# Optimization experiments

Measured on AMD Instinct MI355X. Metric: run time of the kernel, lower is better.

## Reference

```python
import jax, jax.numpy as jnp
import numpy as np

B, T, C, HS = 4, 2048, 1024, 64  # batch, seq, n_embd, head_size


def setup_inputs() -> dict:
    key = jax.random.key(0)
    k1, k2, k3, k4 = jax.random.split(key, 4)
    x = jax.random.normal(k1, (B, T, C), dtype=jnp.float32)
    Wq = jax.random.normal(k2, (HS, C), dtype=jnp.float32) * (C ** -0.5)
    Wk = jax.random.normal(k3, (HS, C), dtype=jnp.float32) * (C ** -0.5)
    Wv = jax.random.normal(k4, (HS, C), dtype=jnp.float32) * (C ** -0.5)
    return {"x": x, "Wq": Wq, "Wk": Wk, "Wv": Wv}


def reference(x, Wq, Wk, Wv):
    # q,k,v: [B,T,HS] (nn.Linear: x @ W.T, no bias)
    q = jnp.einsum('btc,hc->bth', x, Wq)
    k = jnp.einsum('btc,hc->bth', x, Wk)
    v = jnp.einsum('btc,hc->bth', x, Wv)
    scale = k.shape[-1] ** -0.5
    wei = jnp.einsum('bth,bsh->bts', q, k) * scale  # [B,T,T]
    # causal mask (tril == 0 -> -inf)
    mask = jnp.tril(jnp.ones((T, T), dtype=bool))
    wei = jnp.where(mask, wei, -jnp.inf)
    wei = jax.nn.softmax(wei, axis=-1)
    # dropout p=0.0 -> identity
    out = jnp.einsum('bts,bsh->bth', wei, v)  # [B,T,HS]
    return out
```

## Files before the change

kernel.cpp:

```cpp
#include <hip/hip_runtime.h>
#include <hip/hip_bf16.h>

#define BB 4
#define TT 2048
#define CC 1024
#define HSZ 64
#define NTOT 8192

typedef __attribute__((ext_vector_type(8))) short bf16x8;
typedef __attribute__((ext_vector_type(4))) float f32x4;

__device__ __forceinline__ unsigned short f2bf(float x) {
    __hip_bfloat16 h = __float2bfloat16(x);
    return *reinterpret_cast<unsigned short*>(&h);
}
__device__ __forceinline__ float bf2f(unsigned short u) {
    return __uint_as_float(((unsigned int)u) << 16);
}

__global__ __launch_bounds__(256) void convert_w(
    const float* __restrict__ Wq, const float* __restrict__ Wk,
    const float* __restrict__ Wv, unsigned short* __restrict__ Wh) {
    int i = blockIdx.x * 256 + threadIdx.x;
    if (i >= 192 * 1024) return;
    int c = i >> 10, kk = i & 1023;
    float val;
    if (c < 64) val = Wq[(size_t)c * CC + kk] * 0.125f;
    else if (c < 128) val = Wk[(size_t)(c - 64) * CC + kk];
    else val = Wv[(size_t)(c - 128) * CC + kk];
    Wh[i] = f2bf(val);
}

__global__ __launch_bounds__(512, 2) void qkv_mfma(
    const float* __restrict__ x, const unsigned short* __restrict__ Wh,
    unsigned short* __restrict__ qs, unsigned short* __restrict__ ksb,
    unsigned short* __restrict__ vT) {
    __shared__ __align__(16) unsigned char smem[110592];
    unsigned short* Wc = (unsigned short*)smem;
    float* Pt = (float*)smem;

    const int tid = threadIdx.x;
    const int w = tid >> 6, lane = tid & 63;
    const int l16 = lane & 15, quad = lane >> 4;
    const int ms = w & 1, ks = w >> 1;
    const int row0 = blockIdx.x * 32;
    const int Arow = row0 + ms * 16 + l16;

    f32x4 acc[12];
#pragma unroll
    for (int t = 0; t < 12; ++t) acc[t] = (f32x4){0.f, 0.f, 0.f, 0.f};

    for (int ch = 0; ch < 4; ++ch) {
        const int kb = ks * 256 + ch * 64;
        __syncthreads();
        {
            const int gt = tid & 127;
            unsigned short* Wck = Wc + ks * 13824;
#pragma unroll
            for (int it = 0; it < 12; ++it) {
                int e = gt + it * 128;
                int c = e >> 3, g = e & 7;
                *(uint4*)&Wck[c * 72 + g * 8] = *(const uint4*)&Wh[(size_t)c * CC + kb + g * 8];
            }
        }
        const float* xp = x + (size_t)Arow * CC + kb;
        float4 xa = *(const float4*)&xp[quad * 8];
        float4 xb = *(const float4*)&xp[quad * 8 + 4];
        float4 xc = *(const float4*)&xp[32 + quad * 8];
        float4 xd = *(const float4*)&xp[32 + quad * 8 + 4];
        bf16x8 ah0, al0, ah1, al1;
        {
            float v0[8] = {xa.x, xa.y, xa.z, xa.w, xb.x, xb.y, xb.z, xb.w};
            float v1[8] = {xc.x, xc.y, xc.z, xc.w, xd.x, xd.y, xd.z, xd.w};
#pragma unroll
            for (int j = 0; j < 8; ++j) {
                unsigned short h = f2bf(v0[j]);
                ah0[j] = (short)h;
                al0[j] = (short)f2bf(v0[j] - bf2f(h));
                unsigned short h2 = f2bf(v1[j]);
                ah1[j] = (short)h2;
                al1[j] = (short)f2bf(v1[j] - bf2f(h2));
            }
        }
        __syncthreads();
        const unsigned short* Wck = Wc + ks * 13824;
#pragma unroll
        for (int nt = 0; nt < 12; ++nt) {
            bf16x8 b0 = *(const bf16x8*)&Wck[(nt * 16 + l16) * 72 + quad * 8];
            bf16x8 b1 = *(const bf16x8*)&Wck[(nt * 16 + l16) * 72 + 32 + quad * 8];
            f32x4 a = acc[nt];
            a = __builtin_amdgcn_mfma_f32_16x16x32_bf16(ah0, b0, a, 0, 0, 0);
            a = __builtin_amdgcn_mfma_f32_16x16x32_bf16(al0, b0, a, 0, 0, 0);
            a = __builtin_amdgcn_mfma_f32_16x16x32_bf16(ah1, b1, a, 0, 0, 0);
            a = __builtin_amdgcn_mfma_f32_16x16x32_bf16(al1, b1, a, 0, 0, 0);
            acc[nt] = a;
        }
    }
    __syncthreads();
#pragma unroll
    for (int nt = 0; nt < 12; ++nt)
#pragma unroll
        for (int r = 0; r < 4; ++r)
            Pt[((ms * 4 + ks) * 16 + quad * 4 + r) * 196 + nt * 16 + l16] = acc[nt][r];
    __syncthreads();
    for (int e = tid; e < 32 * 192; e += 512) {
        int row = e / 192, col = e - row * 192;
        int m2 = row >> 4, r16 = row & 15;
        float s = 0.f;
#pragma unroll
        for (int kk = 0; kk < 4; ++kk) s += Pt[((m2 * 4 + kk) * 16 + r16) * 196 + col];
        unsigned short h = f2bf(s);
        int grow = row0 + row;
        if (col < 64) qs[(size_t)grow * HSZ + col] = h;
        else if (col < 128) ksb[(size_t)grow * HSZ + (col - 64)] = h;
        else vT[(size_t)(col - 128) * NTOT + grow] = h;
    }
}

__global__ __launch_bounds__(256, 2) void attn_mfma(
    const unsigned short* __restrict__ qs, const unsigned short* __restrict__ ksb,
    const unsigned short* __restrict__ vT, float* __restrict__ out) {
    __shared__ __align__(16) unsigned char smem[18688];
    unsigned short* Ps = (unsigned short*)smem;
    float* Om = (float*)smem;
    float* Lm = (float*)(smem + 17408);

    const int raw = blockIdx.x;
    const int i = (raw < 256) ? raw : 767 - raw;
    const int b = i >> 7;
    const int qt = i & 127;
    const int t0 = qt * 16;
    const int tid = threadIdx.x;
    const int w = tid >> 6, lane = tid & 63;
    const int l16 = lane & 15, quad = lane >> 4;

    const size_t qoff = (size_t)(b * TT + t0 + l16) * HSZ + quad * 8;
    const bf16x8 aq0 = *(const bf16x8*)&qs[qoff];
    const bf16x8 aq1 = *(const bf16x8*)&qs[qoff + 32];

    f32x4 OC[4];
#pragma unroll
    for (int t = 0; t < 4; ++t) OC[t] = (f32x4){0.f, 0.f, 0.f, 0.f};
    float lsum[4] = {0.f, 0.f, 0.f, 0.f};

    const int nk = (qt >> 2) + 1;
    for (int j = w; j < nk; j += 4) {
        const int key0 = j * 64;
        f32x4 S[4];
#pragma unroll
        for (int nt = 0; nt < 4; ++nt) {
            const size_t ko = (size_t)(b * TT + key0 + nt * 16 + l16) * HSZ + quad * 8;
            bf16x8 bk0 = *(const bf16x8*)&ksb[ko];
            bf16x8 bk1 = *(const bf16x8*)&ksb[ko + 32];
            f32x4 a = (f32x4){0.f, 0.f, 0.f, 0.f};
            a = __builtin_amdgcn_mfma_f32_16x16x32_bf16(aq0, bk0, a, 0, 0, 0);
            a = __builtin_amdgcn_mfma_f32_16x16x32_bf16(aq1, bk1, a, 0, 0, 0);
            S[nt] = a;
        }
        if (j == nk - 1) {
#pragma unroll
            for (int nt = 0; nt < 4; ++nt) {
                const int key = key0 + nt * 16 + l16;
#pragma unroll
                for (int r = 0; r < 4; ++r)
                    if (key > t0 + quad * 4 + r) S[nt][r] = -1e30f;
            }
        }
#pragma unroll
        for (int nt = 0; nt < 4; ++nt)
#pragma unroll
            for (int r = 0; r < 4; ++r) S[nt][r] = __expf(S[nt][r]);
#pragma unroll
        for (int r = 0; r < 4; ++r)
            lsum[r] += S[0][r] + S[1][r] + S[2][r] + S[3][r];
        unsigned short* Pw = Ps + w * 1152;
#pragma unroll
        for (int nt = 0; nt < 4; ++nt)
#pragma unroll
            for (int r = 0; r < 4; ++r)
                Pw[(quad * 4 + r) * 72 + nt * 16 + l16] = f2bf(S[nt][r]);
        bf16x8 pf0 = *(const bf16x8*)&Pw[l16 * 72 + quad * 8];
        bf16x8 pf1 = *(const bf16x8*)&Pw[l16 * 72 + 32 + quad * 8];
#pragma unroll
        for (int ht = 0; ht < 4; ++ht) {
            const size_t vo = (size_t)(ht * 16 + l16) * NTOT + b * TT + key0 + quad * 8;
            bf16x8 bv0 = *(const bf16x8*)&vT[vo];
            bf16x8 bv1 = *(const bf16x8*)&vT[vo + 32];
            f32x4 a = OC[ht];
            a = __builtin_amdgcn_mfma_f32_16x16x32_bf16(pf0, bv0, a, 0, 0, 0);
            a = __builtin_amdgcn_mfma_f32_16x16x32_bf16(pf1, bv1, a, 0, 0, 0);
            OC[ht] = a;
        }
    }
#pragma unroll
    for (int r = 0; r < 4; ++r) {
        float v = lsum[r];
#pragma unroll
        for (int off = 1; off < 16; off <<= 1) v += __shfl_xor(v, off, 64);
        lsum[r] = v;
    }
    __syncthreads();
#pragma unroll
    for (int ht = 0; ht < 4; ++ht)
#pragma unroll
        for (int r = 0; r < 4; ++r)
            Om[(w * 16 + quad * 4 + r) * 68 + ht * 16 + l16] = OC[ht][r];
    if (l16 == 0) {
#pragma unroll
        for (int r = 0; r < 4; ++r) Lm[w * 16 + quad * 4 + r] = lsum[r];
    }
    __syncthreads();
    {
        const int row = tid >> 4, h0 = (tid & 15) * 4;
        float L = 0.f, o0 = 0.f, o1 = 0.f, o2 = 0.f, o3 = 0.f;
#pragma unroll
        for (int w2 = 0; w2 < 4; ++w2) {
            L += Lm[w2 * 16 + row];
            const float* p = &Om[(w2 * 16 + row) * 68 + h0];
            o0 += p[0]; o1 += p[1]; o2 += p[2]; o3 += p[3];
        }
        const float inv = 1.f / L;
        *(float4*)&out[(size_t)(b * TT + t0 + row) * HSZ + h0] =
            (float4){o0 * inv, o1 * inv, o2 * inv, o3 * inv};
    }
}

extern "C" void kernel_launch(void* const* d_in, const int* in_sizes, int n_in,
                              void* d_out, int out_size, void* d_ws, size_t ws_size,
                              hipStream_t stream) {
    const float* x  = (const float*)d_in[0];
    const float* Wq = (const float*)d_in[1];
    const float* Wk = (const float*)d_in[2];
    const float* Wv = (const float*)d_in[3];
    float* out = (float*)d_out;

    unsigned short* qs = (unsigned short*)d_ws;
    unsigned short* ksb = qs + (size_t)NTOT * HSZ;
    unsigned short* vT = ksb + (size_t)NTOT * HSZ;
    unsigned short* Wh = vT + (size_t)NTOT * HSZ;

    convert_w<<<768, 256, 0, stream>>>(Wq, Wk, Wv, Wh);
    qkv_mfma<<<256, 512, 0, stream>>>(x, Wh, qs, ksb, vT);
    attn_mfma<<<512, 256, 0, stream>>>(qs, ksb, vT, out);
}
```

Before: 112.2 us.

## Drop LDS weight staging in QKV projection and prefetch K/V in attention

The QKV projection kernel no longer stages weight chunks through shared memory. Each wave reads bf16 weights directly from global/L2, and blocks shrink to 16 rows and 256 threads with twice as many blocks, which removes two barriers per chunk and a large LDS allocation and should allow more occupancy. The attention kernel loads K fragments for the next key tile one iteration ahead and issues V loads before the QK MFMAs, hiding global load latency at the cost of more registers. The attention kernel's shared buffer is also trimmed.

```diff
diff --git a/kernel.cpp b/kernel.cpp
--- a/kernel.cpp
+++ b/kernel.cpp
@@ -31,38 +31,25 @@
     Wh[i] = f2bf(val);
 }
 
-__global__ __launch_bounds__(512, 2) void qkv_mfma(
+__global__ __launch_bounds__(256, 2) void qkv_mfma(
     const float* __restrict__ x, const unsigned short* __restrict__ Wh,
     unsigned short* __restrict__ qs, unsigned short* __restrict__ ksb,
     unsigned short* __restrict__ vT) {
-    __shared__ __align__(16) unsigned char smem[110592];
-    unsigned short* Wc = (unsigned short*)smem;
-    float* Pt = (float*)smem;
+    __shared__ __align__(16) float Pt[4 * 16 * 196];
 
     const int tid = threadIdx.x;
     const int w = tid >> 6, lane = tid & 63;
     const int l16 = lane & 15, quad = lane >> 4;
-    const int ms = w & 1, ks = w >> 1;
-    const int row0 = blockIdx.x * 32;
-    const int Arow = row0 + ms * 16 + l16;
+    const int row0 = blockIdx.x * 16;
+    const int Arow = row0 + l16;
 
     f32x4 acc[12];
 #pragma unroll
     for (int t = 0; t < 12; ++t) acc[t] = (f32x4){0.f, 0.f, 0.f, 0.f};
 
+#pragma unroll
     for (int ch = 0; ch < 4; ++ch) {
-        const int kb = ks * 256 + ch * 64;
-        __syncthreads();
-        {
-            const int gt = tid & 127;
-            unsigned short* Wck = Wc + ks * 13824;
-#pragma unroll
-            for (int it = 0; it < 12; ++it) {
-                int e = gt + it * 128;
-                int c = e >> 3, g = e & 7;
-                *(uint4*)&Wck[c * 72 + g * 8] = *(const uint4*)&Wh[(size_t)c * CC + kb + g * 8];
-            }
-        }
+        const int kb = w * 256 + ch * 64;
         const float* xp = x + (size_t)Arow * CC + kb;
         float4 xa = *(const float4*)&xp[quad * 8];
         float4 xb = *(const float4*)&xp[quad * 8 + 4];
@@ -82,12 +69,11 @@
                 al1[j] = (short)f2bf(v1[j] - bf2f(h2));
             }
         }
-        __syncthreads();
-        const unsigned short* Wck = Wc + ks * 13824;
 #pragma unroll
         for (int nt = 0; nt < 12; ++nt) {
-            bf16x8 b0 = *(const bf16x8*)&Wck[(nt * 16 + l16) * 72 + quad * 8];
-            bf16x8 b1 = *(const bf16x8*)&Wck[(nt * 16 + l16) * 72 + 32 + quad * 8];
+            const unsigned short* Wp = &Wh[(size_t)(nt * 16 + l16) * CC + kb + quad * 8];
+            bf16x8 b0 = *(const bf16x8*)Wp;
+            bf16x8 b1 = *(const bf16x8*)(Wp + 32);
             f32x4 a = acc[nt];
             a = __builtin_amdgcn_mfma_f32_16x16x32_bf16(ah0, b0, a, 0, 0, 0);
             a = __builtin_amdgcn_mfma_f32_16x16x32_bf16(al0, b0, a, 0, 0, 0);
@@ -96,21 +82,19 @@
             acc[nt] = a;
         }
     }
+#pragma unroll
+    for (int nt = 0; nt < 12; ++nt)
+#pragma unroll
+        for (int r = 0; r < 4; ++r)
+            Pt[(w * 16 + quad * 4 + r) * 196 + nt * 16 + l16] = acc[nt][r];
     __syncthreads();
-#pragma unroll
-    for (int nt = 0; nt < 12; ++nt)
-#pragma unroll
-        for (int r = 0; r < 4; ++r)
-            Pt[((ms * 4 + ks) * 16 + quad * 4 + r) * 196 + nt * 16 + l16] = acc[nt][r];
-    __syncthreads();
-    for (int e = tid; e < 32 * 192; e += 512) {
-        int row = e / 192, col = e - row * 192;
-        int m2 = row >> 4, r16 = row & 15;
+    for (int e = tid; e < 16 * 192; e += 256) {
+        const int row = e / 192, col = e - row * 192;
         float s = 0.f;
 #pragma unroll
-        for (int kk = 0; kk < 4; ++kk) s += Pt[((m2 * 4 + kk) * 16 + r16) * 196 + col];
+        for (int kk = 0; kk < 4; ++kk) s += Pt[(kk * 16 + row) * 196 + col];
         unsigned short h = f2bf(s);
-        int grow = row0 + row;
+        const int grow = row0 + row;
         if (col < 64) qs[(size_t)grow * HSZ + col] = h;
         else if (col < 128) ksb[(size_t)grow * HSZ + (col - 64)] = h;
         else vT[(size_t)(col - 128) * NTOT + grow] = h;
@@ -120,7 +104,7 @@
 __global__ __launch_bounds__(256, 2) void attn_mfma(
     const unsigned short* __restrict__ qs, const unsigned short* __restrict__ ksb,
     const unsigned short* __restrict__ vT, float* __restrict__ out) {
-    __shared__ __align__(16) unsigned char smem[18688];
+    __shared__ __align__(16) unsigned char smem[17664];
     unsigned short* Ps = (unsigned short*)smem;
     float* Om = (float*)smem;
     float* Lm = (float*)(smem + 17408);
@@ -143,18 +127,46 @@
     for (int t = 0; t < 4; ++t) OC[t] = (f32x4){0.f, 0.f, 0.f, 0.f};
     float lsum[4] = {0.f, 0.f, 0.f, 0.f};
 
+    const unsigned short* kbase = ksb + (size_t)b * TT * HSZ;
     const int nk = (qt >> 2) + 1;
+
+    bf16x8 ck0[4], ck1[4];
+    if (w < nk) {
+        const int key0 = w * 64;
+#pragma unroll
+        for (int nt = 0; nt < 4; ++nt) {
+            const unsigned short* kp = kbase + (size_t)(key0 + nt * 16 + l16) * HSZ + quad * 8;
+            ck0[nt] = *(const bf16x8*)kp;
+            ck1[nt] = *(const bf16x8*)(kp + 32);
+        }
+    }
+
     for (int j = w; j < nk; j += 4) {
         const int key0 = j * 64;
+        bf16x8 cv0[4], cv1[4];
+#pragma unroll
+        for (int ht = 0; ht < 4; ++ht) {
+            const unsigned short* vp = vT + (size_t)(ht * 16 + l16) * NTOT + b * TT + key0 + quad * 8;
+            cv0[ht] = *(const bf16x8*)vp;
+            cv1[ht] = *(const bf16x8*)(vp + 32);
+        }
+        bf16x8 nk0[4], nk1[4];
+        const bool more = (j + 4) < nk;
+        if (more) {
+            const int key0n = key0 + 256;
+#pragma unroll
+            for (int nt = 0; nt < 4; ++nt) {
+                const unsigned short* kp = kbase + (size_t)(key0n + nt * 16 + l16) * HSZ + quad * 8;
+                nk0[nt] = *(const bf16x8*)kp;
+                nk1[nt] = *(const bf16x8*)(kp + 32);
+            }
+        }
         f32x4 S[4];
 #pragma unroll
         for (int nt = 0; nt < 4; ++nt) {
-            const size_t ko = (size_t)(b * TT + key0 + nt * 16 + l16) * HSZ + quad * 8;
-            bf16x8 bk0 = *(const bf16x8*)&ksb[ko];
-            bf16x8 bk1 = *(const bf16x8*)&ksb[ko + 32];
             f32x4 a = (f32x4){0.f, 0.f, 0.f, 0.f};
-            a = __builtin_amdgcn_mfma_f32_16x16x32_bf16(aq0, bk0, a, 0, 0, 0);
-            a = __builtin_amdgcn_mfma_f32_16x16x32_bf16(aq1, bk1, a, 0, 0, 0);
+            a = __builtin_amdgcn_mfma_f32_16x16x32_bf16(aq0, ck0[nt], a, 0, 0, 0);
+            a = __builtin_amdgcn_mfma_f32_16x16x32_bf16(aq1, ck1[nt], a, 0, 0, 0);
             S[nt] = a;
         }
         if (j == nk - 1) {
@@ -183,13 +195,14 @@
         bf16x8 pf1 = *(const bf16x8*)&Pw[l16 * 72 + 32 + quad * 8];
 #pragma unroll
         for (int ht = 0; ht < 4; ++ht) {
-            const size_t vo = (size_t)(ht * 16 + l16) * NTOT + b * TT + key0 + quad * 8;
-            bf16x8 bv0 = *(const bf16x8*)&vT[vo];
-            bf16x8 bv1 = *(const bf16x8*)&vT[vo + 32];
             f32x4 a = OC[ht];
-            a = __builtin_amdgcn_mfma_f32_16x16x32_bf16(pf0, bv0, a, 0, 0, 0);
-            a = __builtin_amdgcn_mfma_f32_16x16x32_bf16(pf1, bv1, a, 0, 0, 0);
+            a = __builtin_amdgcn_mfma_f32_16x16x32_bf16(pf0, cv0[ht], a, 0, 0, 0);
+            a = __builtin_amdgcn_mfma_f32_16x16x32_bf16(pf1, cv1[ht], a, 0, 0, 0);
             OC[ht] = a;
+        }
+        if (more) {
+#pragma unroll
+            for (int nt = 0; nt < 4; ++nt) { ck0[nt] = nk0[nt]; ck1[nt] = nk1[nt]; }
         }
     }
 #pragma unroll
@@ -240,6 +253,6 @@
     unsigned short* Wh = vT + (size_t)NTOT * HSZ;
 
     convert_w<<<768, 256, 0, stream>>>(Wq, Wk, Wv, Wh);
-    qkv_mfma<<<256, 512, 0, stream>>>(x, Wh, qs, ksb, vT);
+    qkv_mfma<<<512, 256, 0, stream>>>(x, Wh, qs, ksb, vT);
     attn_mfma<<<512, 256, 0, stream>>>(qs, ksb, vT, out);
 }
```

Measured after the change: 120.4 us. 1.07x slower.

## Pre-split x into bf16 hi/lo, drop LDS from QKV GEMM, pair attention key blocks

Applied to the files above, without the earlier changes.

A new conversion kernel splits all of x into bf16 high and low halves in global memory, alongside the weight conversion. The QKV projection is rewritten without shared memory: each wave computes one 16x16 output tile over the full reduction dimension, reading the pre-split x and weights straight from global memory. This removes the LDS staging and the cross-wave split-K reduction. The attention loop now processes two 64-key blocks per iteration to expose more MFMA and load parallelism. The trade-off is an extra full-size write and read of x in bf16, plus higher register pressure in attention.

```diff
diff --git a/kernel.cpp b/kernel.cpp
--- a/kernel.cpp
+++ b/kernel.cpp
@@ -18,109 +18,82 @@
     return __uint_as_float(((unsigned int)u) << 16);
 }
 
-__global__ __launch_bounds__(256) void convert_w(
+__global__ __launch_bounds__(256) void convert_all(
     const float* __restrict__ Wq, const float* __restrict__ Wk,
-    const float* __restrict__ Wv, unsigned short* __restrict__ Wh) {
-    int i = blockIdx.x * 256 + threadIdx.x;
-    if (i >= 192 * 1024) return;
-    int c = i >> 10, kk = i & 1023;
-    float val;
-    if (c < 64) val = Wq[(size_t)c * CC + kk] * 0.125f;
-    else if (c < 128) val = Wk[(size_t)(c - 64) * CC + kk];
-    else val = Wv[(size_t)(c - 128) * CC + kk];
-    Wh[i] = f2bf(val);
-}
-
-__global__ __launch_bounds__(512, 2) void qkv_mfma(
-    const float* __restrict__ x, const unsigned short* __restrict__ Wh,
+    const float* __restrict__ Wv, const float* __restrict__ x,
+    unsigned short* __restrict__ Wh, unsigned short* __restrict__ xh,
+    unsigned short* __restrict__ xl) {
+    const int idx = blockIdx.x * 256 + threadIdx.x;
+    const int stride = 2048 * 256;
+    for (int i = idx; i < 49152; i += stride) {
+        const int c = i >> 8, k4 = i & 255;
+        float4 wv;
+        if (c < 64) {
+            wv = *(const float4*)&Wq[(size_t)c * CC + k4 * 4];
+            wv.x *= 0.125f; wv.y *= 0.125f; wv.z *= 0.125f; wv.w *= 0.125f;
+        } else if (c < 128) {
+            wv = *(const float4*)&Wk[(size_t)(c - 64) * CC + k4 * 4];
+        } else {
+            wv = *(const float4*)&Wv[(size_t)(c - 128) * CC + k4 * 4];
+        }
+        ushort4 h = {f2bf(wv.x), f2bf(wv.y), f2bf(wv.z), f2bf(wv.w)};
+        *(ushort4*)&Wh[(size_t)i * 4] = h;
+    }
+    for (int i = idx; i < 2097152; i += stride) {
+        float4 xv = *(const float4*)&x[(size_t)i * 4];
+        ushort4 h = {f2bf(xv.x), f2bf(xv.y), f2bf(xv.z), f2bf(xv.w)};
+        ushort4 l = {f2bf(xv.x - bf2f(h.x)), f2bf(xv.y - bf2f(h.y)),
+                     f2bf(xv.z - bf2f(h.z)), f2bf(xv.w - bf2f(h.w))};
+        *(ushort4*)&xh[(size_t)i * 4] = h;
+        *(ushort4*)&xl[(size_t)i * 4] = l;
+    }
+}
+
+__global__ __launch_bounds__(768, 4) void qkv_mfma(
+    const unsigned short* __restrict__ xh, const unsigned short* __restrict__ xl,
+    const unsigned short* __restrict__ Wh,
     unsigned short* __restrict__ qs, unsigned short* __restrict__ ksb,
     unsigned short* __restrict__ vT) {
-    __shared__ __align__(16) unsigned char smem[110592];
-    unsigned short* Wc = (unsigned short*)smem;
-    float* Pt = (float*)smem;
-
     const int tid = threadIdx.x;
     const int w = tid >> 6, lane = tid & 63;
     const int l16 = lane & 15, quad = lane >> 4;
-    const int ms = w & 1, ks = w >> 1;
-    const int row0 = blockIdx.x * 32;
-    const int Arow = row0 + ms * 16 + l16;
-
-    f32x4 acc[12];
-#pragma unroll
-    for (int t = 0; t < 12; ++t) acc[t] = (f32x4){0.f, 0.f, 0.f, 0.f};
-
-    for (int ch = 0; ch < 4; ++ch) {
-        const int kb = ks * 256 + ch * 64;
-        __syncthreads();
-        {
-            const int gt = tid & 127;
-            unsigned short* Wck = Wc + ks * 13824;
-#pragma unroll
-            for (int it = 0; it < 12; ++it) {
-                int e = gt + it * 128;
-                int c = e >> 3, g = e & 7;
-                *(uint4*)&Wck[c * 72 + g * 8] = *(const uint4*)&Wh[(size_t)c * CC + kb + g * 8];
-            }
-        }
-        const float* xp = x + (size_t)Arow * CC + kb;
-        float4 xa = *(const float4*)&xp[quad * 8];
-        float4 xb = *(const float4*)&xp[quad * 8 + 4];
-        float4 xc = *(const float4*)&xp[32 + quad * 8];
-        float4 xd = *(const float4*)&xp[32 + quad * 8 + 4];
-        bf16x8 ah0, al0, ah1, al1;
-        {
-            float v0[8] = {xa.x, xa.y, xa.z, xa.w, xb.x, xb.y, xb.z, xb.w};
-            float v1[8] = {xc.x, xc.y, xc.z, xc.w, xd.x, xd.y, xd.z, xd.w};
-#pragma unroll
-            for (int j = 0; j < 8; ++j) {
-                unsigned short h = f2bf(v0[j]);
-                ah0[j] = (short)h;
-                al0[j] = (short)f2bf(v0[j] - bf2f(h));
-                unsigned short h2 = f2bf(v1[j]);
-                ah1[j] = (short)h2;
-                al1[j] = (short)f2bf(v1[j] - bf2f(h2));
-            }
-        }
-        __syncthreads();
-        const unsigned short* Wck = Wc + ks * 13824;
-#pragma unroll
-        for (int nt = 0; nt < 12; ++nt) {
-            bf16x8 b0 = *(const bf16x8*)&Wck[(nt * 16 + l16) * 72 + quad * 8];
-            bf16x8 b1 = *(const bf16x8*)&Wck[(nt * 16 + l16) * 72 + 32 + quad * 8];
-            f32x4 a = acc[nt];
-            a = __builtin_amdgcn_mfma_f32_16x16x32_bf16(ah0, b0, a, 0, 0, 0);
-            a = __builtin_amdgcn_mfma_f32_16x16x32_bf16(al0, b0, a, 0, 0, 0);
-            a = __builtin_amdgcn_mfma_f32_16x16x32_bf16(ah1, b1, a, 0, 0, 0);
-            a = __builtin_amdgcn_mfma_f32_16x16x32_bf16(al1, b1, a, 0, 0, 0);
-            acc[nt] = a;
-        }
-    }
-    __syncthreads();
-#pragma unroll
-    for (int nt = 0; nt < 12; ++nt)
+    const int row0 = blockIdx.x * 16;
+
+    const unsigned short* xhp = xh + (size_t)(row0 + l16) * CC;
+    const unsigned short* xlp = xl + (size_t)(row0 + l16) * CC;
+    const unsigned short* Wp = Wh + (size_t)(w * 16 + l16) * CC;
+
+    f32x4 acc = (f32x4){0.f, 0.f, 0.f, 0.f};
+#pragma unroll
+    for (int ch = 0; ch < 16; ++ch) {
+        const int kb = ch * 64 + quad * 8;
+        bf16x8 ah0 = *(const bf16x8*)&xhp[kb];
+        bf16x8 ah1 = *(const bf16x8*)&xhp[kb + 32];
+        bf16x8 al0 = *(const bf16x8*)&xlp[kb];
+        bf16x8 al1 = *(const bf16x8*)&xlp[kb + 32];
+        bf16x8 b0 = *(const bf16x8*)&Wp[kb];
+        bf16x8 b1 = *(const bf16x8*)&Wp[kb + 32];
+        acc = __builtin_amdgcn_mfma_f32_16x16x32_bf16(ah0, b0, acc, 0, 0, 0);
+        acc = __builtin_amdgcn_mfma_f32_16x16x32_bf16(al0, b0, acc, 0, 0, 0);
+        acc = __builtin_amdgcn_mfma_f32_16x16x32_bf16(ah1, b1, acc, 0, 0, 0);
+        acc = __builtin_amdgcn_mfma_f32_16x16x32_bf16(al1, b1, acc, 0, 0, 0);
+    }
+    const int col = w * 16 + l16;
+    if (col < 128) {
+        unsigned short* dst = (col < 64) ? (qs + col) : (ksb + (col - 64));
 #pragma unroll
         for (int r = 0; r < 4; ++r)
-            Pt[((ms * 4 + ks) * 16 + quad * 4 + r) * 196 + nt * 16 + l16] = acc[nt][r];
-    __syncthreads();
-    for (int e = tid; e < 32 * 192; e += 512) {
-        int row = e / 192, col = e - row * 192;
-        int m2 = row >> 4, r16 = row & 15;
-        float s = 0.f;
-#pragma unroll
-        for (int kk = 0; kk < 4; ++kk) s += Pt[((m2 * 4 + kk) * 16 + r16) * 196 + col];
-        unsigned short h = f2bf(s);
-        int grow = row0 + row;
-        if (col < 64) qs[(size_t)grow * HSZ + col] = h;
-        else if (col < 128) ksb[(size_t)grow * HSZ + (col - 64)] = h;
-        else vT[(size_t)(col - 128) * NTOT + grow] = h;
+            dst[(size_t)(row0 + quad * 4 + r) * HSZ] = f2bf(acc[r]);
+    } else {
+        ushort4 pk = {f2bf(acc[0]), f2bf(acc[1]), f2bf(acc[2]), f2bf(acc[3])};
+        *(ushort4*)&vT[(size_t)(col - 128) * NTOT + row0 + quad * 4] = pk;
     }
 }
 
 __global__ __launch_bounds__(256, 2) void attn_mfma(
     const unsigned short* __restrict__ qs, const unsigned short* __restrict__ ksb,
     const unsigned short* __restrict__ vT, float* __restrict__ out) {
-    __shared__ __align__(16) unsigned char smem[18688];
+    __shared__ __align__(16) unsigned char smem[18432];
     unsigned short* Ps = (unsigned short*)smem;
     float* Om = (float*)smem;
     float* Lm = (float*)(smem + 17408);
@@ -143,52 +116,94 @@
     for (int t = 0; t < 4; ++t) OC[t] = (f32x4){0.f, 0.f, 0.f, 0.f};
     float lsum[4] = {0.f, 0.f, 0.f, 0.f};
 
+    const unsigned short* kbase = ksb + (size_t)b * TT * HSZ;
     const int nk = (qt >> 2) + 1;
-    for (int j = w; j < nk; j += 4) {
-        const int key0 = j * 64;
-        f32x4 S[4];
+
+    for (int jp = w * 2; jp < nk; jp += 8) {
+        const int j0 = jp, j1 = jp + 1;
+        const bool v1 = (j1 < nk);
+        const int key0 = j0 * 64;
+        const int key1 = v1 ? j1 * 64 : key0;
+
+        f32x4 S0[4], S1[4];
 #pragma unroll
         for (int nt = 0; nt < 4; ++nt) {
-            const size_t ko = (size_t)(b * TT + key0 + nt * 16 + l16) * HSZ + quad * 8;
-            bf16x8 bk0 = *(const bf16x8*)&ksb[ko];
-            bf16x8 bk1 = *(const bf16x8*)&ksb[ko + 32];
+            const unsigned short* kp0 = kbase + (size_t)(key0 + nt * 16 + l16) * HSZ + quad * 8;
+            const unsigned short* kp1 = kbase + (size_t)(key1 + nt * 16 + l16) * HSZ + quad * 8;
+            bf16x8 k00 = *(const bf16x8*)kp0;
+            bf16x8 k01 = *(const bf16x8*)(kp0 + 32);
+            bf16x8 k10 = *(const bf16x8*)kp1;
+            bf16x8 k11 = *(const bf16x8*)(kp1 + 32);
             f32x4 a = (f32x4){0.f, 0.f, 0.f, 0.f};
-            a = __builtin_amdgcn_mfma_f32_16x16x32_bf16(aq0, bk0, a, 0, 0, 0);
-            a = __builtin_amdgcn_mfma_f32_16x16x32_bf16(aq1, bk1, a, 0, 0, 0);
-            S[nt] = a;
-        }
-        if (j == nk - 1) {
+            a = __builtin_amdgcn_mfma_f32_16x16x32_bf16(aq0, k00, a, 0, 0, 0);
+            a = __builtin_amdgcn_mfma_f32_16x16x32_bf16(aq1, k01, a, 0, 0, 0);
+            S0[nt] = a;
+            f32x4 c = (f32x4){0.f, 0.f, 0.f, 0.f};
+            c = __builtin_amdgcn_mfma_f32_16x16x32_bf16(aq0, k10, c, 0, 0, 0);
+            c = __builtin_amdgcn_mfma_f32_16x16x32_bf16(aq1, k11, c, 0, 0, 0);
+            S1[nt] = c;
+        }
+        if (j0 == nk - 1) {
 #pragma unroll
             for (int nt = 0; nt < 4; ++nt) {
                 const int key = key0 + nt * 16 + l16;
 #pragma unroll
                 for (int r = 0; r < 4; ++r)
-                    if (key > t0 + quad * 4 + r) S[nt][r] = -1e30f;
+                    if (key > t0 + quad * 4 + r) S0[nt][r] = -1e30f;
+            }
+        }
+        if (!v1) {
+#pragma unroll
+            for (int nt = 0; nt < 4; ++nt)
+#pragma unroll
+                for (int r = 0; r < 4; ++r) S1[nt][r] = -1e30f;
+        } else if (j1 == nk - 1) {
+#pragma unroll
+            for (int nt = 0; nt < 4; ++nt) {
+                const int key = key1 + nt * 16 + l16;
+#pragma unroll
+                for (int r = 0; r < 4; ++r)
+                    if (key > t0 + quad * 4 + r) S1[nt][r] = -1e30f;
             }
         }
 #pragma unroll
         for (int nt = 0; nt < 4; ++nt)
 #pragma unroll
-            for (int r = 0; r < 4; ++r) S[nt][r] = __expf(S[nt][r]);
+            for (int r = 0; r < 4; ++r) {
+                S0[nt][r] = __expf(S0[nt][r]);
+                S1[nt][r] = __expf(S1[nt][r]);
+            }
 #pragma unroll
         for (int r = 0; r < 4; ++r)
-            lsum[r] += S[0][r] + S[1][r] + S[2][r] + S[3][r];
-        unsigned short* Pw = Ps + w * 1152;
+            lsum[r] += S0[0][r] + S0[1][r] + S0[2][r] + S0[3][r] +
+                       S1[0][r] + S1[1][r] + S1[2][r] + S1[3][r];
+        unsigned short* Pw = Ps + w * 2304;
 #pragma unroll
         for (int nt = 0; nt < 4; ++nt)
 #pragma unroll
-            for (int r = 0; r < 4; ++r)
-                Pw[(quad * 4 + r) * 72 + nt * 16 + l16] = f2bf(S[nt][r]);
-        bf16x8 pf0 = *(const bf16x8*)&Pw[l16 * 72 + quad * 8];
-        bf16x8 pf1 = *(const bf16x8*)&Pw[l16 * 72 + 32 + quad * 8];
+            for (int r = 0; r < 4; ++r) {
+                Pw[(quad * 4 + r) * 72 + nt * 16 + l16] = f2bf(S0[nt][r]);
+                Pw[1152 + (quad * 4 + r) * 72 + nt * 16 + l16] = f2bf(S1[nt][r]);
+            }
+        bf16x8 p00 = *(const bf16x8*)&Pw[l16 * 72 + quad * 8];
+        bf16x8 p01 = *(const bf16x8*)&Pw[l16 * 72 + 32 + quad * 8];
+        bf16x8 p10 = *(const bf16x8*)&Pw[1152 + l16 * 72 + quad * 8];
+        bf16x8 p11 = *(const bf16x8*)&Pw[1152 + l16 * 72 + 32 + quad * 8];
 #pragma unroll
         for (int ht = 0; ht < 4; ++ht) {
-            const size_t vo = (size_t)(ht * 16 + l16) * NTOT + b * TT + key0 + quad * 8;
-            bf16x8 bv0 = *(const bf16x8*)&vT[vo];
-            bf16x8 bv1 = *(const bf16x8*)&vT[vo + 32];
+            const unsigned short* vp0 =
+                vT + (size_t)(ht * 16 + l16) * NTOT + b * TT + key0 + quad * 8;
+            const unsigned short* vp1 =
+                vT + (size_t)(ht * 16 + l16) * NTOT + b * TT + key1 + quad * 8;
+            bf16x8 v00 = *(const bf16x8*)vp0;
+            bf16x8 v01 = *(const bf16x8*)(vp0 + 32);
+            bf16x8 v10 = *(const bf16x8*)vp1;
+            bf16x8 v11 = *(const bf16x8*)(vp1 + 32);
             f32x4 a = OC[ht];
-            a = __builtin_amdgcn_mfma_f32_16x16x32_bf16(pf0, bv0, a, 0, 0, 0);
-            a = __builtin_amdgcn_mfma_f32_16x16x32_bf16(pf1, bv1, a, 0, 0, 0);
+            a = __builtin_amdgcn_mfma_f32_16x16x32_bf16(p00, v00, a, 0, 0, 0);
+            a = __builtin_amdgcn_mfma_f32_16x16x32_bf16(p01, v01, a, 0, 0, 0);
+            a = __builtin_amdgcn_mfma_f32_16x16x32_bf16(p10, v10, a, 0, 0, 0);
+            a = __builtin_amdgcn_mfma_f32_16x16x32_bf16(p11, v11, a, 0, 0, 0);
             OC[ht] = a;
         }
     }
@@ -238,8 +253,10 @@
     unsigned short* ksb = qs + (size_t)NTOT * HSZ;
     unsigned short* vT = ksb + (size_t)NTOT * HSZ;
     unsigned short* Wh = vT + (size_t)NTOT * HSZ;
-
-    convert_w<<<768, 256, 0, stream>>>(Wq, Wk, Wv, Wh);
-    qkv_mfma<<<256, 512, 0, stream>>>(x, Wh, qs, ksb, vT);
+    unsigned short* xh = Wh + (size_t)192 * CC;
+    unsigned short* xl = xh + (size_t)NTOT * CC;
+
+    convert_all<<<2048, 256, 0, stream>>>(Wq, Wk, Wv, x, Wh, xh, xl);
+    qkv_mfma<<<512, 768, 0, stream>>>(xh, xl, Wh, qs, ksb, vT);
     attn_mfma<<<512, 256, 0, stream>>>(qs, ksb, vT, out);
 }
```

After: 170.1 us. +51.6%, slower.
